# Performance work log

Hardware: AMD Instinct MI355X
Metric: run time of the kernel (lower is better)

Reference implementation:

```python
import jax, jax.numpy as jnp
import numpy as np

N = 170000      # nodes
E = 2400000     # edges
F_IN = 128      # dataset.num_features
H = 64          # hidden_channels
C = 40          # dataset.num_classes
L = 8           # num_layers
ENTROPY = 1.0   # args.entropy
EPS = 1e-20


def setup_inputs() -> dict:
    key = jax.random.key(0)
    ks = jax.random.split(key, 10)
    x = jax.random.normal(ks[0], (N, F_IN), jnp.float32)
    edge_src = jax.random.randint(ks[1], (E,), 0, N)
    edge_dst = jax.random.randint(ks[2], (E,), 0, N)
    edge_weight = jax.random.uniform(ks[3], (E,), jnp.float32) / 14.0  # ~1/deg scale
    u = jax.random.uniform(ks[4], (N, L + 1), jnp.float32, 1e-6, 1.0 - 1e-6)
    gumbel = -jnp.log(-jnp.log(u))  # standard Gumbel noise for gumbel_softmax
    lin0_w = jax.random.normal(ks[5], (F_IN, H), jnp.float32) / np.float32(np.sqrt(F_IN))
    lin0_b = jnp.zeros((H,), jnp.float32)
    meta_w = jax.random.normal(ks[6], (H, 1), jnp.float32) / np.float32(np.sqrt(H))
    meta_b = jnp.zeros((1,), jnp.float32)
    lin1_w = jax.random.normal(ks[7], (H, C), jnp.float32) / np.float32(np.sqrt(H))
    lin1_b = jnp.zeros((C,), jnp.float32)
    return dict(x=x, edge_weight=edge_weight, gumbel=gumbel,
                lin0_w=lin0_w, lin0_b=lin0_b, meta_w=meta_w, meta_b=meta_b,
                lin1_w=lin1_w, lin1_b=lin1_b,
                edge_src=edge_src, edge_dst=edge_dst)


def reference(x, edge_weight, gumbel, lin0_w, lin0_b, meta_w, meta_b,
              lin1_w, lin1_b, edge_src, edge_dst):
    # input projection + relu (dropout=0 -> no-op)
    x = jnp.maximum(x @ lin0_w + lin0_b, 0.0)  # [N,H]
    xs = [x]
    # GCNII layers with conv.alpha = conv.beta = 0 -> pure edge-weighted
    # scatter-add propagation followed by relu.
    for _ in range(L):
        msg = edge_weight[:, None] * x[edge_src]              # [E,H] gather
        x = jax.ops.segment_sum(msg, edge_dst, num_segments=N)  # [N,H] scatter-add
        x = jnp.maximum(x, 0.0)
        xs.append(x)
    xMat = jnp.stack(xs, axis=1)  # [N, L+1, H] (preds == xMatrix since concat='none')
    # MetaNet: [N, L+1]
    r = jnp.squeeze(xMat @ meta_w, -1) + meta_b[0]
    # get_t: stick-breaking with sigmoid; last column uses t=1 times cumprod
    s = jax.nn.sigmoid(r)                                    # [N, L+1]
    cp_excl = jnp.concatenate(
        [jnp.ones((N, 1), s.dtype), jnp.cumprod(1.0 - s, axis=1)[:, :-1]], axis=1)
    t = s * cp_excl
    t = t.at[:, -1].set(cp_excl[:, -1])
    ent_loss = ENTROPY * (-(jnp.log(t + EPS) * t).sum(1).mean())
    # gumbel_softmax(log(t+eps), tau=1, hard=False)
    tM = jax.nn.softmax(jnp.log(t + EPS) + gumbel, axis=1)   # [N, L+1]
    # layer mixing: [N,1,L+1] @ [N,L+1,H] -> [N,H]
    out = jnp.einsum('nl,nlh->nh', tM, xMat)
    out = out @ lin1_w + lin1_b
    return jax.nn.log_softmax(out, axis=-1), ent_loss
```

## Files before the change

### kernel.cpp

```cpp
#include <hip/hip_runtime.h>
#include <hip/hip_bf16.h>

#define N_NODES 170000
#define N_EDGES 2400000
#define F_IN_   128
#define H_      64
#define C_OUT   40
#define L_LAYERS 8
#define LP1     9
#define EPS_T   1e-20f
#define ROW_ELEMS (LP1 * H_)

typedef unsigned short u16;

__device__ __forceinline__ float bf2f(u16 u) {
    union { unsigned int i; float f; } c; c.i = ((unsigned int)u) << 16; return c.f;
}
__device__ __forceinline__ u16 f2bf(float f) {
    __hip_bfloat16 h = __float2bfloat16(f);
    return *reinterpret_cast<u16*>(&h);
}

__device__ __forceinline__ float waveReduceSum(float v) {
    for (int m = 32; m; m >>= 1) v += __shfl_xor(v, m, 64);
    return v;
}
__device__ __forceinline__ float waveReduceMax(float v) {
    for (int m = 32; m; m >>= 1) v = fmaxf(v, __shfl_xor(v, m, 64));
    return v;
}

__global__ __launch_bounds__(256) void k_zero4(float4* __restrict__ p) {
    p[blockIdx.x * 256 + threadIdx.x] = make_float4(0.f, 0.f, 0.f, 0.f);
}

__global__ __launch_bounds__(256) void k_hist(
    const int* __restrict__ edst, int* __restrict__ deg)
{
    int e = blockIdx.x * 256 + threadIdx.x;
    if (e < N_EDGES) atomicAdd(&deg[edst[e]], 1);
}

#define SCAN_TPB 256
#define SCAN_VPT 8
#define SCAN_EPB (SCAN_TPB * SCAN_VPT)
#define SCAN_BLOCKS ((N_NODES + SCAN_EPB - 1) / SCAN_EPB)

__global__ __launch_bounds__(SCAN_TPB) void k_scan1(
    const int* __restrict__ deg, int* __restrict__ rowstart,
    int* __restrict__ blockSums)
{
    __shared__ int tsum[SCAN_TPB];
    int tid = threadIdx.x;
    int base = blockIdx.x * SCAN_EPB + tid * SCAN_VPT;
    int vals[SCAN_VPT];
    int local = 0;
    #pragma unroll
    for (int i = 0; i < SCAN_VPT; ++i) {
        int idx = base + i;
        int v = (idx < N_NODES) ? deg[idx] : 0;
        vals[i] = local;
        local += v;
    }
    tsum[tid] = local;
    __syncthreads();
    for (int off = 1; off < SCAN_TPB; off <<= 1) {
        int v = (tid >= off) ? tsum[tid - off] : 0;
        __syncthreads();
        tsum[tid] += v;
        __syncthreads();
    }
    int texcl = tsum[tid] - local;
    #pragma unroll
    for (int i = 0; i < SCAN_VPT; ++i) {
        int idx = base + i;
        if (idx < N_NODES) rowstart[idx] = texcl + vals[i];
    }
    if (tid == SCAN_TPB - 1) blockSums[blockIdx.x] = tsum[tid];
}

__global__ __launch_bounds__(64) void k_scan2(int* __restrict__ blockSums) {
    if (threadIdx.x == 0) {
        int acc = 0;
        for (int i = 0; i < SCAN_BLOCKS; ++i) {
            int v = blockSums[i];
            blockSums[i] = acc;
            acc += v;
        }
    }
}

__global__ __launch_bounds__(SCAN_TPB) void k_scan3(
    int* __restrict__ rowstart, const int* __restrict__ blockSums)
{
    int off = blockSums[blockIdx.x];
    int base = blockIdx.x * SCAN_EPB + threadIdx.x * SCAN_VPT;
    #pragma unroll
    for (int i = 0; i < SCAN_VPT; ++i) {
        int idx = base + i;
        if (idx < N_NODES) rowstart[idx] += off;
    }
}

__global__ __launch_bounds__(256) void k_bucket(
    const int* __restrict__ esrc, const int* __restrict__ edst,
    const float* __restrict__ ew, const int* __restrict__ rowstart,
    int* __restrict__ cursor, int2* __restrict__ csr)
{
    int e = blockIdx.x * 256 + threadIdx.x;
    if (e >= N_EDGES) return;
    int d = edst[e];
    int p = rowstart[d] + atomicAdd(&cursor[d], 1);
    csr[p] = make_int2(esrc[e], __float_as_int(ew[e]));
}

#define L0_NPB 64
__global__ __launch_bounds__(256) void k_lin0(
    const float* __restrict__ x, const float* __restrict__ W0,
    const float* __restrict__ b0, const float* __restrict__ mw,
    const float* __restrict__ mb, u16* __restrict__ xMatB,
    float* __restrict__ r)
{
    __shared__ float Wt[H_ * F_IN_];
    __shared__ float xr[L0_NPB * F_IN_];
    int tid = threadIdx.x;
    for (int i = tid; i < F_IN_ * H_; i += 256) {
        int k = i >> 6, c = i & 63;
        Wt[c * F_IN_ + (k ^ ((c & 7) << 2))] = W0[i];
    }
    int nb = blockIdx.x * L0_NPB;
    const float4* x4 = (const float4*)(x + (size_t)nb * F_IN_);
    float4* xr4 = (float4*)xr;
    int nvalid = N_NODES - nb; if (nvalid > L0_NPB) nvalid = L0_NPB;
    int limit4 = nvalid * (F_IN_ / 4);
    for (int i = tid; i < L0_NPB * (F_IN_ / 4); i += 256)
        xr4[i] = (i < limit4) ? x4[i] : make_float4(0.f, 0.f, 0.f, 0.f);
    __syncthreads();

    int wave = tid >> 6, lane = tid & 63;
    const int mbase = wave * 16;
    float bias = b0[lane];
    float acc[16];
    #pragma unroll
    for (int j = 0; j < 16; ++j) acc[j] = bias;
    const int wrow = lane * F_IN_;
    const int wsw = (lane & 7) << 2;
    for (int k0 = 0; k0 < F_IN_; k0 += 4) {
        float4 wv = *(const float4*)&Wt[wrow + (k0 ^ wsw)];
        #pragma unroll
        for (int j = 0; j < 16; ++j) {
            float4 xv = *(const float4*)&xr[(mbase + j) * F_IN_ + k0];
            acc[j] = fmaf(xv.w, wv.w,
                     fmaf(xv.z, wv.z, fmaf(xv.y, wv.y, fmaf(xv.x, wv.x, acc[j]))));
        }
    }
    float mwv = mw[lane];
    for (int j = 0; j < 16; ++j) {
        int n = nb + mbase + j;
        if (n >= N_NODES) break;
        float v = fmaxf(acc[j], 0.f);
        xMatB[(size_t)n * ROW_ELEMS + lane] = f2bf(v);
        float pr = waveReduceSum(v * mwv);
        if (lane == 0) r[n * LP1] = pr + mb[0];
    }
}

__global__ __launch_bounds__(256) void k_prop(
    const u16* __restrict__ xMatB, int l,
    const int* __restrict__ rowstart, const int* __restrict__ deg,
    const int2* __restrict__ csr,
    const float* __restrict__ mw, const float* __restrict__ mb,
    u16* __restrict__ xMatOut, float* __restrict__ r)
{
    int tid = threadIdx.x, wave = tid >> 6, lane = tid & 63;
    int n = blockIdx.x * 4 + wave;
    int sl = lane & 15, q = lane >> 4;
    int start = rowstart[n];
    int d = deg[n];

    int myS = 0; float myW = 0.f;
    if (lane < d) {
        int2 e = csr[start + lane];
        myS = e.x; myW = __int_as_float(e.y);
    }
    const unsigned loff = (unsigned)l * H_ + sl * 4;
    float a0 = 0.f, a1 = 0.f, a2 = 0.f, a3 = 0.f;
    float c0 = 0.f, c1 = 0.f, c2 = 0.f, c3 = 0.f;
    int dmax = (d < 64) ? d : 64;
    for (int kb = 0; kb < dmax; kb += 8) {
        int idx0 = kb + q;
        int idx1 = kb + q + 4;
        int   s0 = __shfl(myS, idx0, 64);
        float w0 = __shfl(myW, idx0, 64);
        int   s1 = __shfl(myS, idx1, 64);
        float w1 = __shfl(myW, idx1, 64);
        ushort4 v0 = *reinterpret_cast<const ushort4*>(
            &xMatB[(size_t)(unsigned)s0 * ROW_ELEMS + loff]);
        ushort4 v1 = *reinterpret_cast<const ushort4*>(
            &xMatB[(size_t)(unsigned)s1 * ROW_ELEMS + loff]);
        a0 = fmaf(bf2f(v0.x), w0, a0);
        a1 = fmaf(bf2f(v0.y), w0, a1);
        a2 = fmaf(bf2f(v0.z), w0, a2);
        a3 = fmaf(bf2f(v0.w), w0, a3);
        c0 = fmaf(bf2f(v1.x), w1, c0);
        c1 = fmaf(bf2f(v1.y), w1, c1);
        c2 = fmaf(bf2f(v1.z), w1, c2);
        c3 = fmaf(bf2f(v1.w), w1, c3);
    }
    for (int kb = 64; kb < d; kb += 4) {
        int idx = kb + q;
        if (idx < d) {
            int2 e = csr[start + idx];
            float w = __int_as_float(e.y);
            ushort4 v = *reinterpret_cast<const ushort4*>(
                &xMatB[(size_t)(unsigned)e.x * ROW_ELEMS + loff]);
            a0 = fmaf(bf2f(v.x), w, a0);
            a1 = fmaf(bf2f(v.y), w, a1);
            a2 = fmaf(bf2f(v.z), w, a2);
            a3 = fmaf(bf2f(v.w), w, a3);
        }
    }
    a0 += c0; a1 += c1; a2 += c2; a3 += c3;
    a0 += __shfl_xor(a0, 16, 64); a0 += __shfl_xor(a0, 32, 64);
    a1 += __shfl_xor(a1, 16, 64); a1 += __shfl_xor(a1, 32, 64);
    a2 += __shfl_xor(a2, 16, 64); a2 += __shfl_xor(a2, 32, 64);
    a3 += __shfl_xor(a3, 16, 64); a3 += __shfl_xor(a3, 32, 64);
    a0 = fmaxf(a0, 0.f); a1 = fmaxf(a1, 0.f);
    a2 = fmaxf(a2, 0.f); a3 = fmaxf(a3, 0.f);
    if (q == 0) {
        ushort4 o; o.x = f2bf(a0); o.y = f2bf(a1); o.z = f2bf(a2); o.w = f2bf(a3);
        *reinterpret_cast<ushort4*>(
            &xMatOut[(size_t)n * ROW_ELEMS + (l + 1) * H_ + sl * 4]) = o;
    }
    float dot = a0 * mw[4 * sl] + a1 * mw[4 * sl + 1] +
                a2 * mw[4 * sl + 2] + a3 * mw[4 * sl + 3];
    float pr = waveReduceSum(dot) * 0.25f;
    if (lane == 0) r[n * LP1 + (l + 1)] = pr + mb[0];
}

__global__ __launch_bounds__(256) void k_gate(
    const float* __restrict__ r, const float* __restrict__ gum,
    float* __restrict__ tM, float* __restrict__ entPart)
{
    __shared__ float lds[4];
    int tid = threadIdx.x;
    int n = blockIdx.x * 256 + tid;
    float ent = 0.f;
    if (n < N_NODES) {
        float t[LP1], lg[LP1];
        float cp = 1.f;
        #pragma unroll
        for (int j = 0; j < LP1; ++j) {
            float rv = r[n * LP1 + j];
            float s = 1.f / (1.f + expf(-rv));
            t[j] = (j == L_LAYERS) ? cp : s * cp;
            cp *= (1.f - s);
        }
        float mx = -INFINITY;
        #pragma unroll
        for (int j = 0; j < LP1; ++j) {
            float lt = logf(t[j] + EPS_T);
            ent -= t[j] * lt;
            lg[j] = lt + gum[n * LP1 + j];
            mx = fmaxf(mx, lg[j]);
        }
        float se = 0.f;
        #pragma unroll
        for (int j = 0; j < LP1; ++j) { lg[j] = expf(lg[j] - mx); se += lg[j]; }
        float inv = 1.f / se;
        #pragma unroll
        for (int j = 0; j < LP1; ++j) tM[n * LP1 + j] = lg[j] * inv;
    }
    float s = waveReduceSum(ent);
    int wave = tid >> 6, lane = tid & 63;
    if (lane == 0) lds[wave] = s;
    __syncthreads();
    if (tid == 0) entPart[blockIdx.x] = lds[0] + lds[1] + lds[2] + lds[3];
}

__global__ __launch_bounds__(256) void k_final(
    const u16* __restrict__ xMatB, const float* __restrict__ tM,
    const float* __restrict__ W1, const float* __restrict__ b1,
    float* __restrict__ out)
{
    __shared__ float mixLds[4][H_];
    int tid = threadIdx.x, wave = tid >> 6, lane = tid & 63;
    int n = blockIdx.x * 4 + wave;
    float tm = (lane < LP1) ? tM[n * LP1 + lane] : 0.f;
    float m = 0.f;
    #pragma unroll
    for (int j = 0; j < LP1; ++j) {
        float w = __shfl(tm, j, 64);
        m = fmaf(w, bf2f(xMatB[(size_t)n * ROW_ELEMS + j * H_ + lane]), m);
    }
    mixLds[wave][lane] = m;
    __syncthreads();
    float o = -INFINITY;
    if (lane < C_OUT) {
        float a = b1[lane];
        #pragma unroll 8
        for (int h = 0; h < H_; ++h)
            a = fmaf(mixLds[wave][h], W1[h * C_OUT + lane], a);
        o = a;
    }
    float omx = waveReduceMax(o);
    float ex = (lane < C_OUT) ? expf(o - omx) : 0.f;
    float es = waveReduceSum(ex);
    if (lane < C_OUT)
        out[(size_t)n * C_OUT + lane] = o - omx - logf(es);
}

__global__ __launch_bounds__(256) void k_entreduce(
    const float* __restrict__ part, int n, float scale, float* __restrict__ out)
{
    __shared__ float lds[4];
    int tid = threadIdx.x;
    float s = 0.f;
    for (int i = tid; i < n; i += 256) s += part[i];
    s = waveReduceSum(s);
    int wave = tid >> 6, lane = tid & 63;
    if (lane == 0) lds[wave] = s;
    __syncthreads();
    if (tid == 0) out[0] = (lds[0] + lds[1] + lds[2] + lds[3]) * scale;
}

extern "C" void kernel_launch(void* const* d_in, const int* in_sizes, int n_in,
                              void* d_out, int out_size, void* d_ws, size_t ws_size,
                              hipStream_t stream)
{
    const float* x   = (const float*)d_in[0];
    const float* ew  = (const float*)d_in[1];
    const float* gum = (const float*)d_in[2];
    const float* W0  = (const float*)d_in[3];
    const float* b0  = (const float*)d_in[4];
    const float* mw  = (const float*)d_in[5];
    const float* mb  = (const float*)d_in[6];
    const float* W1  = (const float*)d_in[7];
    const float* b1  = (const float*)d_in[8];
    const int* esrc  = (const int*)d_in[9];
    const int* edst  = (const int*)d_in[10];
    float* out = (float*)d_out;

    const size_t xMatBytes = (size_t)N_NODES * ROW_ELEMS * sizeof(u16);
    const size_t rBytes    = (size_t)N_NODES * LP1 * sizeof(float);
    const size_t tMBytes   = (size_t)N_NODES * LP1 * sizeof(float);
    const size_t entBytes  = (size_t)((N_NODES + 255) / 256) * sizeof(float);
    const size_t degBytes  = (size_t)N_NODES * sizeof(int);
    const size_t curBytes  = (size_t)N_NODES * sizeof(int);
    const size_t rowBytes  = (size_t)N_NODES * sizeof(int);
    const size_t bsBytes   = 512;
    const size_t csrBytes  = (size_t)N_EDGES * sizeof(int2);
    const size_t need = xMatBytes + rBytes + tMBytes + entBytes + degBytes +
                        curBytes + rowBytes + bsBytes + csrBytes;
    if (ws_size < need) return;

    char* p = (char*)d_ws;
    u16*  xMatB    = (u16*)p;           p += xMatBytes;
    float* rbuf    = (float*)p;         p += rBytes;
    float* tMbuf   = (float*)p;         p += tMBytes;
    float* entP    = (float*)p;         p += entBytes;
    int*  deg      = (int*)p;           p += degBytes;
    int*  cursor   = (int*)p;           p += curBytes;
    int*  rowstart = (int*)p;           p += rowBytes;
    int*  blockSums= (int*)p;           p += bsBytes;
    int2* csr      = (int2*)p;

    const int nodeBlocks = N_NODES / 4;
    const int edgeBlocks = (N_EDGES + 255) / 256;
    const int gateBlocks = (N_NODES + 255) / 256;
    const int lin0Blocks = (N_NODES + L0_NPB - 1) / L0_NPB;

    k_zero4<<<333, 256, 0, stream>>>((float4*)deg);
    k_hist<<<edgeBlocks, 256, 0, stream>>>(edst, deg);
    k_scan1<<<SCAN_BLOCKS, SCAN_TPB, 0, stream>>>(deg, rowstart, blockSums);
    k_scan2<<<1, 64, 0, stream>>>(blockSums);
    k_scan3<<<SCAN_BLOCKS, SCAN_TPB, 0, stream>>>(rowstart, blockSums);
    k_bucket<<<edgeBlocks, 256, 0, stream>>>(esrc, edst, ew, rowstart, cursor, csr);

    k_lin0<<<lin0Blocks, 256, 0, stream>>>(x, W0, b0, mw, mb, xMatB, rbuf);
    for (int l = 0; l < L_LAYERS; ++l)
        k_prop<<<nodeBlocks, 256, 0, stream>>>(xMatB, l, rowstart, deg, csr,
                                               mw, mb, xMatB, rbuf);
    k_gate<<<gateBlocks, 256, 0, stream>>>(rbuf, gum, tMbuf, entP);
    k_final<<<nodeBlocks, 256, 0, stream>>>(xMatB, tMbuf, W1, b1, out);
    k_entreduce<<<1, 256, 0, stream>>>(entP, gateBlocks, 1.0f / N_NODES,
                                       out + (size_t)N_NODES * C_OUT);
}
```

Measured before the change: 993.3 us.

## Unroll prop gather to four edges per step and partition CSR bucketing by destination range

The propagation kernel now processes four edges per iteration per quarter-wave, with clamped shuffle indices and zeroed weights in place of bounds checks, so more independent gather loads are in flight. The final meta-dot reduction is shortened to a 16-lane reduction. CSR bucketing is split into eight passes over all edges, each handling one destination range, so atomic and scattered writes stay in a smaller address window for better cache locality. In exchange the edge arrays are read eight times, and low-degree nodes issue wasted padded loads.

```diff
diff --git a/kernel.cpp b/kernel.cpp
--- a/kernel.cpp
+++ b/kernel.cpp
@@ -105,11 +105,12 @@
 __global__ __launch_bounds__(256) void k_bucket(
     const int* __restrict__ esrc, const int* __restrict__ edst,
     const float* __restrict__ ew, const int* __restrict__ rowstart,
-    int* __restrict__ cursor, int2* __restrict__ csr)
+    int* __restrict__ cursor, int2* __restrict__ csr, int lo, int hi)
 {
     int e = blockIdx.x * 256 + threadIdx.x;
     if (e >= N_EDGES) return;
     int d = edst[e];
+    if (d < lo || d >= hi) return;
     int p = rowstart[d] + atomicAdd(&cursor[d], 1);
     csr[p] = make_int2(esrc[e], __float_as_int(ew[e]));
 }
@@ -177,6 +178,7 @@
     int sl = lane & 15, q = lane >> 4;
     int start = rowstart[n];
     int d = deg[n];
+    int dm1 = (d > 0) ? (d - 1) : 0;
 
     int myS = 0; float myW = 0.f;
     if (lane < d) {
@@ -184,58 +186,89 @@
         myS = e.x; myW = __int_as_float(e.y);
     }
     const unsigned loff = (unsigned)l * H_ + sl * 4;
-    float a0 = 0.f, a1 = 0.f, a2 = 0.f, a3 = 0.f;
-    float c0 = 0.f, c1 = 0.f, c2 = 0.f, c3 = 0.f;
+
+    float a0x = 0.f, a0y = 0.f, a0z = 0.f, a0w = 0.f;
+    float a1x = 0.f, a1y = 0.f, a1z = 0.f, a1w = 0.f;
+    float a2x = 0.f, a2y = 0.f, a2z = 0.f, a2w = 0.f;
+    float a3x = 0.f, a3y = 0.f, a3z = 0.f, a3w = 0.f;
+
     int dmax = (d < 64) ? d : 64;
-    for (int kb = 0; kb < dmax; kb += 8) {
+    int kb = 0;
+    do {
         int idx0 = kb + q;
         int idx1 = kb + q + 4;
-        int   s0 = __shfl(myS, idx0, 64);
-        float w0 = __shfl(myW, idx0, 64);
-        int   s1 = __shfl(myS, idx1, 64);
-        float w1 = __shfl(myW, idx1, 64);
+        int idx2 = kb + q + 8;
+        int idx3 = kb + q + 12;
+        int ic0 = (idx0 < dm1) ? idx0 : dm1;
+        int ic1 = (idx1 < dm1) ? idx1 : dm1;
+        int ic2 = (idx2 < dm1) ? idx2 : dm1;
+        int ic3 = (idx3 < dm1) ? idx3 : dm1;
+        int   s0 = __shfl(myS, ic0, 64); float w0 = __shfl(myW, ic0, 64);
+        int   s1 = __shfl(myS, ic1, 64); float w1 = __shfl(myW, ic1, 64);
+        int   s2 = __shfl(myS, ic2, 64); float w2 = __shfl(myW, ic2, 64);
+        int   s3 = __shfl(myS, ic3, 64); float w3 = __shfl(myW, ic3, 64);
+        if (idx0 >= d) w0 = 0.f;
+        if (idx1 >= d) w1 = 0.f;
+        if (idx2 >= d) w2 = 0.f;
+        if (idx3 >= d) w3 = 0.f;
         ushort4 v0 = *reinterpret_cast<const ushort4*>(
             &xMatB[(size_t)(unsigned)s0 * ROW_ELEMS + loff]);
         ushort4 v1 = *reinterpret_cast<const ushort4*>(
             &xMatB[(size_t)(unsigned)s1 * ROW_ELEMS + loff]);
-        a0 = fmaf(bf2f(v0.x), w0, a0);
-        a1 = fmaf(bf2f(v0.y), w0, a1);
-        a2 = fmaf(bf2f(v0.z), w0, a2);
-        a3 = fmaf(bf2f(v0.w), w0, a3);
-        c0 = fmaf(bf2f(v1.x), w1, c0);
-        c1 = fmaf(bf2f(v1.y), w1, c1);
-        c2 = fmaf(bf2f(v1.z), w1, c2);
-        c3 = fmaf(bf2f(v1.w), w1, c3);
-    }
-    for (int kb = 64; kb < d; kb += 4) {
-        int idx = kb + q;
-        if (idx < d) {
-            int2 e = csr[start + idx];
-            float w = __int_as_float(e.y);
-            ushort4 v = *reinterpret_cast<const ushort4*>(
-                &xMatB[(size_t)(unsigned)e.x * ROW_ELEMS + loff]);
-            a0 = fmaf(bf2f(v.x), w, a0);
-            a1 = fmaf(bf2f(v.y), w, a1);
-            a2 = fmaf(bf2f(v.z), w, a2);
-            a3 = fmaf(bf2f(v.w), w, a3);
+        ushort4 v2 = *reinterpret_cast<const ushort4*>(
+            &xMatB[(size_t)(unsigned)s2 * ROW_ELEMS + loff]);
+        ushort4 v3 = *reinterpret_cast<const ushort4*>(
+            &xMatB[(size_t)(unsigned)s3 * ROW_ELEMS + loff]);
+        a0x = fmaf(bf2f(v0.x), w0, a0x); a0y = fmaf(bf2f(v0.y), w0, a0y);
+        a0z = fmaf(bf2f(v0.z), w0, a0z); a0w = fmaf(bf2f(v0.w), w0, a0w);
+        a1x = fmaf(bf2f(v1.x), w1, a1x); a1y = fmaf(bf2f(v1.y), w1, a1y);
+        a1z = fmaf(bf2f(v1.z), w1, a1z); a1w = fmaf(bf2f(v1.w), w1, a1w);
+        a2x = fmaf(bf2f(v2.x), w2, a2x); a2y = fmaf(bf2f(v2.y), w2, a2y);
+        a2z = fmaf(bf2f(v2.z), w2, a2z); a2w = fmaf(bf2f(v2.w), w2, a2w);
+        a3x = fmaf(bf2f(v3.x), w3, a3x); a3y = fmaf(bf2f(v3.y), w3, a3y);
+        a3z = fmaf(bf2f(v3.z), w3, a3z); a3w = fmaf(bf2f(v3.w), w3, a3w);
+        kb += 16;
+    } while (kb < dmax);
+
+    for (int kb2 = 64; kb2 < d; kb2 += 16) {
+        #pragma unroll
+        for (int j = 0; j < 4; ++j) {
+            int idx = kb2 + j * 4 + q;
+            if (idx < d) {
+                int2 e = csr[start + idx];
+                float w = __int_as_float(e.y);
+                ushort4 v = *reinterpret_cast<const ushort4*>(
+                    &xMatB[(size_t)(unsigned)e.x * ROW_ELEMS + loff]);
+                a0x = fmaf(bf2f(v.x), w, a0x);
+                a0y = fmaf(bf2f(v.y), w, a0y);
+                a0z = fmaf(bf2f(v.z), w, a0z);
+                a0w = fmaf(bf2f(v.w), w, a0w);
+            }
         }
     }
-    a0 += c0; a1 += c1; a2 += c2; a3 += c3;
-    a0 += __shfl_xor(a0, 16, 64); a0 += __shfl_xor(a0, 32, 64);
-    a1 += __shfl_xor(a1, 16, 64); a1 += __shfl_xor(a1, 32, 64);
-    a2 += __shfl_xor(a2, 16, 64); a2 += __shfl_xor(a2, 32, 64);
-    a3 += __shfl_xor(a3, 16, 64); a3 += __shfl_xor(a3, 32, 64);
-    a0 = fmaxf(a0, 0.f); a1 = fmaxf(a1, 0.f);
-    a2 = fmaxf(a2, 0.f); a3 = fmaxf(a3, 0.f);
+
+    float r0 = a0x + a1x + a2x + a3x;
+    float r1 = a0y + a1y + a2y + a3y;
+    float r2 = a0z + a1z + a2z + a3z;
+    float r3 = a0w + a1w + a2w + a3w;
+    r0 += __shfl_xor(r0, 16, 64); r0 += __shfl_xor(r0, 32, 64);
+    r1 += __shfl_xor(r1, 16, 64); r1 += __shfl_xor(r1, 32, 64);
+    r2 += __shfl_xor(r2, 16, 64); r2 += __shfl_xor(r2, 32, 64);
+    r3 += __shfl_xor(r3, 16, 64); r3 += __shfl_xor(r3, 32, 64);
+    r0 = fmaxf(r0, 0.f); r1 = fmaxf(r1, 0.f);
+    r2 = fmaxf(r2, 0.f); r3 = fmaxf(r3, 0.f);
     if (q == 0) {
-        ushort4 o; o.x = f2bf(a0); o.y = f2bf(a1); o.z = f2bf(a2); o.w = f2bf(a3);
+        ushort4 o; o.x = f2bf(r0); o.y = f2bf(r1); o.z = f2bf(r2); o.w = f2bf(r3);
         *reinterpret_cast<ushort4*>(
             &xMatOut[(size_t)n * ROW_ELEMS + (l + 1) * H_ + sl * 4]) = o;
     }
-    float dot = a0 * mw[4 * sl] + a1 * mw[4 * sl + 1] +
-                a2 * mw[4 * sl + 2] + a3 * mw[4 * sl + 3];
-    float pr = waveReduceSum(dot) * 0.25f;
-    if (lane == 0) r[n * LP1 + (l + 1)] = pr + mb[0];
+    float dot = r0 * mw[4 * sl] + r1 * mw[4 * sl + 1] +
+                r2 * mw[4 * sl + 2] + r3 * mw[4 * sl + 3];
+    dot += __shfl_xor(dot, 1, 64);
+    dot += __shfl_xor(dot, 2, 64);
+    dot += __shfl_xor(dot, 4, 64);
+    dot += __shfl_xor(dot, 8, 64);
+    if (lane == 0) r[n * LP1 + (l + 1)] = dot + mb[0];
 }
 
 __global__ __launch_bounds__(256) void k_gate(
@@ -375,7 +408,11 @@
     k_scan1<<<SCAN_BLOCKS, SCAN_TPB, 0, stream>>>(deg, rowstart, blockSums);
     k_scan2<<<1, 64, 0, stream>>>(blockSums);
     k_scan3<<<SCAN_BLOCKS, SCAN_TPB, 0, stream>>>(rowstart, blockSums);
-    k_bucket<<<edgeBlocks, 256, 0, stream>>>(esrc, edst, ew, rowstart, cursor, csr);
+    const int STEP = N_NODES / 8;
+    for (int i = 0; i < 8; ++i)
+        k_bucket<<<edgeBlocks, 256, 0, stream>>>(esrc, edst, ew, rowstart,
+                                                 cursor, csr, i * STEP,
+                                                 (i + 1) * STEP);
 
     k_lin0<<<lin0Blocks, 256, 0, stream>>>(x, W0, b0, mw, mb, xMatB, rbuf);
     for (int l = 0; l < L_LAYERS; ++l)
```

Result: faster. 958.3 us (-3.5%).
